# Performance work log

Measured on AMD Instinct MI355X. Metric: run time of the kernel, lower is better.

## Reference

```python
import jax, jax.numpy as jnp
import numpy as np

K = 500        # conv kernel == stride (non-overlapping windows)
C_IN = 8       # embedding dim
C_OUT = 128    # conv out channels
VOCAB = 257    # 256 byte values + padding idx 256


def setup_inputs() -> dict:
    key = jax.random.key(0)
    ks = jax.random.split(key, 10)
    B, L = 8, 1 << 20
    x = jax.random.randint(ks[0], (B, L), 0, VOCAB, dtype=jnp.int32)
    emb = 0.1 * jax.random.normal(ks[1], (VOCAB, C_IN), jnp.float32)
    emb = emb.at[VOCAB - 1].set(0.0)  # padding_idx=256 -> zero row
    lim_c = 1.0 / np.sqrt(C_IN * K)
    w1 = jax.random.uniform(ks[2], (C_OUT, C_IN, K), jnp.float32, -lim_c, lim_c)
    b1 = jax.random.uniform(ks[3], (C_OUT,), jnp.float32, -lim_c, lim_c)
    w2 = jax.random.uniform(ks[4], (C_OUT, C_IN, K), jnp.float32, -lim_c, lim_c)
    b2 = jax.random.uniform(ks[5], (C_OUT,), jnp.float32, -lim_c, lim_c)
    lim_d = 1.0 / np.sqrt(C_OUT)
    wd1 = jax.random.uniform(ks[6], (C_OUT, C_OUT), jnp.float32, -lim_d, lim_d)
    bd1 = jax.random.uniform(ks[7], (C_OUT,), jnp.float32, -lim_d, lim_d)
    wd2 = jax.random.uniform(ks[8], (1, C_OUT), jnp.float32, -lim_d, lim_d)
    bd2 = jax.random.uniform(ks[9], (1,), jnp.float32, -lim_d, lim_d)
    return {"x": x, "emb": emb, "w1": w1, "b1": b1, "w2": w2, "b2": b2,
            "wd1": wd1, "bd1": bd1, "wd2": wd2, "bd2": bd2}


def reference(x, emb, w1, b1, w2, b2, wd1, bd1, wd2, bd2):
    B, L = x.shape
    T = (L - K) // K + 1  # valid conv output length (== L // K here)
    xe = emb[x]                                  # [B, L, 8]  embedding lookup
    win = xe[:, : T * K].reshape(B, T, K, C_IN)  # [B, T, 500, 8] non-overlap windows
    c1 = jnp.einsum('btke,oek->bto', win, w1) + b1  # [B, T, 128]
    c2 = jnp.einsum('btke,oek->bto', win, w2) + b2
    gated = jax.nn.relu(c1) * jax.nn.sigmoid(c2)    # gated activation
    pooled = jnp.max(gated, axis=1)                 # global max pool over time -> [B, 128]
    h = jax.nn.relu(pooled @ wd1.T + bd1)           # [B, 128]
    out = jax.nn.sigmoid(h @ wd2.T + bd2)           # [B, 1]
    return out
```

## Files before the change

kernel.cpp:

```cpp
#include <hip/hip_runtime.h>

#define BATCH   8
#define LSEQ    1048576
#define KCONV   500
#define TWIN    2097
#define MROWS   16776
#define KDIM    4000
#define NDIM    256
#define COUT    128
#define VOCAB   257
#define VOCABP  256

#define BMR     80
#define NTILE   210
#define SLABP   20
#define NSLAB   25
#define NG      125
#define PLANE   (NDIM * 32)
#define AROWSH  168
#define STAGEN  (BMR * SLABP)

#define WTF_OFF   0ull
#define WTF_BYTES ((size_t)NG * PLANE * 2)
#define POOL_OFF  (WTF_OFF + WTF_BYTES)

typedef __attribute__((ext_vector_type(8))) __bf16 bf16x8;
typedef __attribute__((ext_vector_type(4))) float  floatx4;

__device__ inline unsigned short f2bf(float f) {
    union { float f; unsigned u; } c; c.f = f;
    return (unsigned short)((c.u + 0x7FFFu + ((c.u >> 16) & 1u)) >> 16);
}
__device__ inline unsigned pack2(float lo, float hi) {
    return (unsigned)f2bf(lo) | ((unsigned)f2bf(hi) << 16);
}

#define LDS_BARRIER() asm volatile("s_waitcnt lgkmcnt(0)\n\ts_barrier" ::: "memory")

__global__ __launch_bounds__(256) void wprep_kernel(const float* __restrict__ w1,
                                                    const float* __restrict__ w2,
                                                    unsigned short* __restrict__ Wtf,
                                                    float* __restrict__ pool) {
    const int n   = blockIdx.x;
    const int tid = threadIdx.x;
    __shared__ float tile[KDIM];
    const float* src = (n < COUT) ? (w1 + (size_t)n * KDIM)
                                  : (w2 + (size_t)(n - COUT) * KDIM);
    for (int i = tid; i < KDIM; i += 256) tile[i] = src[i];
    __syncthreads();
    for (int i = tid; i < KDIM; i += 256) {
        int g = i >> 5, kk = i & 31;
        Wtf[(size_t)g * PLANE + n * 32 + kk] = f2bf(tile[(i & 7) * KCONV + (i >> 3)]);
    }
    if (n == 0 && tid < BATCH * COUT / 2)
        ((float2*)pool)[tid] = float2{0.f, 0.f};
}

template<int ROWT, int RBASE>
__device__ __forceinline__ void gemm_path(
    const unsigned short* __restrict__ Wtf,
    const float* __restrict__ b1, const float* __restrict__ b2,
    float* __restrict__ pool,
    unsigned short* AsBase, const unsigned short* tableL,
    const int* const (&xptr)[4], const int (&loff)[4], const bool (&sval)[4],
    int tid, int m0)
{
    const int lane = tid & 63;
    const int r16  = lane & 15;
    const int q    = lane >> 4;
    const int cg   = (tid >> 6) & 3;

    const int o0 = cg * 32 + r16;
    const int o1 = o0 + 16;

    const size_t boff[4] = {
        (size_t)o0 * 32 + q * 8,
        (size_t)(o0 + 128) * 32 + q * 8,
        (size_t)o1 * 32 + q * 8,
        (size_t)(o1 + 128) * 32 + q * 8
    };

    floatx4 acc[ROWT][4];
#pragma unroll
    for (int i = 0; i < ROWT; ++i)
#pragma unroll
        for (int j = 0; j < 4; ++j) acc[i][j] = floatx4{0, 0, 0, 0};

    int xv[4], xn[4];
#pragma unroll
    for (int l = 0; l < 4; ++l) xv[l] = sval[l] ? xptr[l][0] : VOCABP;
    __syncthreads();

#pragma unroll
    for (int l = 0; l < 4; ++l) {
        if (l == 3 && tid >= STAGEN - 3 * 512) break;
        uint4 g = *(const uint4*)(tableL + xv[l] * 8);
        *(uint4*)(AsBase + loff[l]) = g;
    }
#pragma unroll
    for (int l = 0; l < 4; ++l) xv[l] = sval[l] ? xptr[l][SLABP] : VOCABP;
    LDS_BARRIER();

    bf16x8 bc0[4], bc1[4], bc2[4] = {};
#pragma unroll
    for (int j = 0; j < 4; ++j) {
        bc0[j] = *(const bf16x8*)(Wtf + boff[j]);
        bc1[j] = *(const bf16x8*)(Wtf + PLANE + boff[j]);
    }

    int buf = 0;
    for (int s = 0; s < NSLAB; ++s) {
        if (s + 2 < NSLAB) {
#pragma unroll
            for (int l = 0; l < 4; ++l)
                xn[l] = sval[l] ? xptr[l][(s + 2) * SLABP] : VOCABP;
        }

        const unsigned short* Asb = AsBase + buf * (BMR * AROWSH);
#pragma unroll
        for (int kt = 0; kt < 5; ++kt) {
            const int g = s * 5 + kt;
            if (g + 2 < NG) {
                const unsigned short* Wp = Wtf + (size_t)(g + 2) * PLANE;
#pragma unroll
                for (int j = 0; j < 4; ++j)
                    bc2[j] = *(const bf16x8*)(Wp + boff[j]);
            }
            bf16x8 af[ROWT];
#pragma unroll
            for (int i = 0; i < ROWT; ++i)
                af[i] = *(const bf16x8*)(Asb + ((RBASE + i) * 16 + r16) * AROWSH
                                         + (kt * 4 + q) * 8);
#pragma unroll
            for (int i = 0; i < ROWT; ++i) {
#pragma unroll
                for (int j = 0; j < 4; ++j)
                    acc[i][j] = __builtin_amdgcn_mfma_f32_16x16x32_bf16(
                        af[i], bc0[j], acc[i][j], 0, 0, 0);
            }
#pragma unroll
            for (int j = 0; j < 4; ++j) { bc0[j] = bc1[j]; bc1[j] = bc2[j]; }
        }

        if (s + 1 < NSLAB) {
            unsigned short* d = AsBase + (buf ^ 1) * (BMR * AROWSH);
#pragma unroll
            for (int l = 0; l < 4; ++l) {
                if (l == 3 && tid >= STAGEN - 3 * 512) break;
                uint4 g = *(const uint4*)(tableL + xv[l] * 8);
                *(uint4*)(d + loff[l]) = g;
            }
        }
#pragma unroll
        for (int l = 0; l < 4; ++l) xv[l] = xn[l];
        LDS_BARRIER();
        buf ^= 1;
    }

    const float b10 = b1[o0], b20 = b2[o0];
    const float b11 = b1[o1], b21 = b2[o1];
    float cur0 = 0.0f, cur1 = 0.0f;
    int curb = (m0 + RBASE * 16 + q * 4) / TWIN;
#pragma unroll
    for (int i = 0; i < ROWT; ++i) {
#pragma unroll
        for (int rg = 0; rg < 4; ++rg) {
            const int row = m0 + (RBASE + i) * 16 + q * 4 + rg;
            if (row < MROWS) {
                const int bb = row / TWIN;
                if (bb != curb) {
                    atomicMax((int*)&pool[curb * COUT + o0], __float_as_int(cur0));
                    atomicMax((int*)&pool[curb * COUT + o1], __float_as_int(cur1));
                    cur0 = 0.0f; cur1 = 0.0f; curb = bb;
                }
                {
                    const float c1 = acc[i][0][rg] + b10;
                    const float c2 = acc[i][1][rg] + b20;
                    cur0 = fmaxf(cur0, fmaxf(c1, 0.0f) / (1.0f + __expf(-c2)));
                }
                {
                    const float c1 = acc[i][2][rg] + b11;
                    const float c2 = acc[i][3][rg] + b21;
                    cur1 = fmaxf(cur1, fmaxf(c1, 0.0f) / (1.0f + __expf(-c2)));
                }
            }
        }
    }
    atomicMax((int*)&pool[curb * COUT + o0], __float_as_int(cur0));
    atomicMax((int*)&pool[curb * COUT + o1], __float_as_int(cur1));
}

__global__ __launch_bounds__(512) void gemm_kernel(const int* __restrict__ x,
                                                   const float* __restrict__ emb,
                                                   const unsigned short* __restrict__ Wtf,
                                                   const float* __restrict__ b1,
                                                   const float* __restrict__ b2,
                                                   float* __restrict__ pool) {
    __shared__ unsigned short tableL[VOCAB * 8];
    __shared__ unsigned short As[2][BMR * AROWSH];

    const int tid = threadIdx.x;
    const int m0  = blockIdx.x * BMR;

    if (tid < VOCAB) {
        const float4* er = (const float4*)(emb + tid * 8);
        float4 a = er[0], b = er[1];
        uint4 u;
        u.x = pack2(a.x, a.y); u.y = pack2(a.z, a.w);
        u.z = pack2(b.x, b.y); u.w = pack2(b.z, b.w);
        *(uint4*)(tableL + tid * 8) = u;
    }

    const int* xptr[4];
    int        loff[4];
    bool       sval[4];
#pragma unroll
    for (int l = 0; l < 4; ++l) {
        int idx = tid + 512 * l;
        sval[l] = (idx < STAGEN);
        int ic  = sval[l] ? idx : 0;
        int row = ic / SLABP;
        int pos = ic - row * SLABP;
        int am  = m0 + row;
        bool av = sval[l] && (am < MROWS);
        sval[l] = av;
        int amc = av ? am : 0;
        int b   = amc / TWIN;
        int t   = amc - b * TWIN;
        xptr[l] = x + ((size_t)b * LSEQ + (size_t)t * KCONV + pos);
        loff[l] = row * AROWSH + pos * 8;
    }

    if (tid < 256)
        gemm_path<3, 0>(Wtf, b1, b2, pool, (unsigned short*)As, tableL,
                        xptr, loff, sval, tid, m0);
    else
        gemm_path<2, 3>(Wtf, b1, b2, pool, (unsigned short*)As, tableL,
                        xptr, loff, sval, tid, m0);
}

__global__ __launch_bounds__(128) void head_kernel(const float* __restrict__ pool,
                                                   const float* __restrict__ wd1,
                                                   const float* __restrict__ bd1,
                                                   const float* __restrict__ wd2,
                                                   const float* __restrict__ bd2,
                                                   float* __restrict__ out) {
    __shared__ float red[BATCH][COUT];
    int j = threadIdx.x;
    float wj = wd2[j];
#pragma unroll
    for (int b = 0; b < BATCH; ++b) {
        float s = bd1[j];
        for (int i = 0; i < COUT; ++i) s += pool[b * COUT + i] * wd1[j * COUT + i];
        red[b][j] = fmaxf(s, 0.0f) * wj;
    }
    __syncthreads();
    if (j < BATCH) {
        float s = 0.0f;
        for (int i = 0; i < COUT; ++i) s += red[j][i];
        out[j] = 1.0f / (1.0f + expf(-(s + bd2[0])));
    }
}

extern "C" void kernel_launch(void* const* d_in, const int* in_sizes, int n_in,
                              void* d_out, int out_size, void* d_ws, size_t ws_size,
                              hipStream_t stream) {
    const int*   x   = (const int*)d_in[0];
    const float* emb = (const float*)d_in[1];
    const float* w1  = (const float*)d_in[2];
    const float* b1  = (const float*)d_in[3];
    const float* w2  = (const float*)d_in[4];
    const float* b2  = (const float*)d_in[5];
    const float* wd1 = (const float*)d_in[6];
    const float* bd1 = (const float*)d_in[7];
    const float* wd2 = (const float*)d_in[8];
    const float* bd2 = (const float*)d_in[9];
    float* out = (float*)d_out;

    unsigned short* Wtf  = (unsigned short*)((char*)d_ws + WTF_OFF);
    float*          pool = (float*)((char*)d_ws + POOL_OFF);

    wprep_kernel<<<dim3(NDIM), dim3(256), 0, stream>>>(w1, w2, Wtf, pool);
    gemm_kernel<<<dim3(NTILE), dim3(512), 0, stream>>>(x, emb, Wtf, b1, b2, pool);
    head_kernel<<<dim3(1), dim3(128), 0, stream>>>(pool, wd1, bd1, wd2, bd2, out);
}
```

Before: 190.8 us.

## Fuse head into GEMM via last-block counter and interleave LDS staging with MFMA

Removes the separate head kernel launch: each GEMM block atomically increments a counter, and the last block reads the pooled maxima and computes the dense head. The embedding-table staging of the next slab is spread across the MFMA k-steps instead of done as a block after them, so LDS traffic overlaps with matrix math. It also adds launch bounds with a minimum of 2 blocks per CU, which may constrain register allocation. The fused head relies on relaxed atomics and a vmcnt wait for ordering.

```diff
diff --git a/kernel.cpp b/kernel.cpp
--- a/kernel.cpp
+++ b/kernel.cpp
@@ -23,6 +23,7 @@
 #define WTF_OFF   0ull
 #define WTF_BYTES ((size_t)NG * PLANE * 2)
 #define POOL_OFF  (WTF_OFF + WTF_BYTES)
+#define CNT_OFF   (POOL_OFF + 4096)
 
 typedef __attribute__((ext_vector_type(8))) __bf16 bf16x8;
 typedef __attribute__((ext_vector_type(4))) float  floatx4;
@@ -40,7 +41,8 @@
 __global__ __launch_bounds__(256) void wprep_kernel(const float* __restrict__ w1,
                                                     const float* __restrict__ w2,
                                                     unsigned short* __restrict__ Wtf,
-                                                    float* __restrict__ pool) {
+                                                    float* __restrict__ pool,
+                                                    int* __restrict__ cnt) {
     const int n   = blockIdx.x;
     const int tid = threadIdx.x;
     __shared__ float tile[KDIM];
@@ -52,8 +54,10 @@
         int g = i >> 5, kk = i & 31;
         Wtf[(size_t)g * PLANE + n * 32 + kk] = f2bf(tile[(i & 7) * KCONV + (i >> 3)]);
     }
-    if (n == 0 && tid < BATCH * COUT / 2)
-        ((float2*)pool)[tid] = float2{0.f, 0.f};
+    if (n == 0) {
+        if (tid < 256) ((float4*)pool)[tid] = float4{0.f, 0.f, 0.f, 0.f};
+        if (tid == 0) *cnt = 0;
+    }
 }
 
 template<int ROWT, int RBASE>
@@ -63,7 +67,7 @@
     float* __restrict__ pool,
     unsigned short* AsBase, const unsigned short* tableL,
     const int* const (&xptr)[4], const int (&loff)[4], const bool (&sval)[4],
-    int tid, int m0)
+    const bool (&sact)[4], int tid, int m0)
 {
     const int lane = tid & 63;
     const int r16  = lane & 15;
@@ -93,9 +97,10 @@
 
 #pragma unroll
     for (int l = 0; l < 4; ++l) {
-        if (l == 3 && tid >= STAGEN - 3 * 512) break;
-        uint4 g = *(const uint4*)(tableL + xv[l] * 8);
-        *(uint4*)(AsBase + loff[l]) = g;
+        if (sact[l]) {
+            uint4 g = *(const uint4*)(tableL + xv[l] * 8);
+            *(uint4*)(AsBase + loff[l]) = g;
+        }
     }
 #pragma unroll
     for (int l = 0; l < 4; ++l) xv[l] = sval[l] ? xptr[l][SLABP] : VOCABP;
@@ -116,7 +121,11 @@
                 xn[l] = sval[l] ? xptr[l][(s + 2) * SLABP] : VOCABP;
         }
 
-        const unsigned short* Asb = AsBase + buf * (BMR * AROWSH);
+        const unsigned short* Asb  = AsBase + buf * (BMR * AROWSH);
+        unsigned short*       dstS = AsBase + (buf ^ 1) * (BMR * AROWSH);
+        const bool stg = (s + 1 < NSLAB);
+        uint4 gr[4];
+
 #pragma unroll
         for (int kt = 0; kt < 5; ++kt) {
             const int g = s * 5 + kt;
@@ -131,6 +140,10 @@
             for (int i = 0; i < ROWT; ++i)
                 af[i] = *(const bf16x8*)(Asb + ((RBASE + i) * 16 + r16) * AROWSH
                                          + (kt * 4 + q) * 8);
+
+            if (kt < 4 && stg && sact[kt])
+                gr[kt] = *(const uint4*)(tableL + xv[kt] * 8);
+
 #pragma unroll
             for (int i = 0; i < ROWT; ++i) {
 #pragma unroll
@@ -140,16 +153,9 @@
             }
 #pragma unroll
             for (int j = 0; j < 4; ++j) { bc0[j] = bc1[j]; bc1[j] = bc2[j]; }
-        }
-
-        if (s + 1 < NSLAB) {
-            unsigned short* d = AsBase + (buf ^ 1) * (BMR * AROWSH);
-#pragma unroll
-            for (int l = 0; l < 4; ++l) {
-                if (l == 3 && tid >= STAGEN - 3 * 512) break;
-                uint4 g = *(const uint4*)(tableL + xv[l] * 8);
-                *(uint4*)(d + loff[l]) = g;
-            }
+
+            if (kt >= 1 && stg && sact[kt - 1])
+                *(uint4*)(dstS + loff[kt - 1]) = gr[kt - 1];
         }
 #pragma unroll
         for (int l = 0; l < 4; ++l) xv[l] = xn[l];
@@ -190,14 +196,20 @@
     atomicMax((int*)&pool[curb * COUT + o1], __float_as_int(cur1));
 }
 
-__global__ __launch_bounds__(512) void gemm_kernel(const int* __restrict__ x,
-                                                   const float* __restrict__ emb,
-                                                   const unsigned short* __restrict__ Wtf,
-                                                   const float* __restrict__ b1,
-                                                   const float* __restrict__ b2,
-                                                   float* __restrict__ pool) {
-    __shared__ unsigned short tableL[VOCAB * 8];
-    __shared__ unsigned short As[2][BMR * AROWSH];
+__global__ __launch_bounds__(512, 2) void gemm_kernel(const int* __restrict__ x,
+                                                      const float* __restrict__ emb,
+                                                      const unsigned short* __restrict__ Wtf,
+                                                      const float* __restrict__ b1,
+                                                      const float* __restrict__ b2,
+                                                      float* __restrict__ pool,
+                                                      int* __restrict__ cnt,
+                                                      const float* __restrict__ wd1,
+                                                      const float* __restrict__ bd1,
+                                                      const float* __restrict__ wd2,
+                                                      const float* __restrict__ bd2,
+                                                      float* __restrict__ out) {
+    __shared__ __align__(16) unsigned short tableL[VOCAB * 8];
+    __shared__ __align__(16) unsigned short As[2][BMR * AROWSH];
 
     const int tid = threadIdx.x;
     const int m0  = blockIdx.x * BMR;
@@ -214,8 +226,10 @@
     const int* xptr[4];
     int        loff[4];
     bool       sval[4];
+    bool       sact[4];
 #pragma unroll
     for (int l = 0; l < 4; ++l) {
+        sact[l] = (l < 3) || (tid < STAGEN - 3 * 512);
         int idx = tid + 512 * l;
         sval[l] = (idx < STAGEN);
         int ic  = sval[l] ? idx : 0;
@@ -233,32 +247,44 @@
 
     if (tid < 256)
         gemm_path<3, 0>(Wtf, b1, b2, pool, (unsigned short*)As, tableL,
-                        xptr, loff, sval, tid, m0);
+                        xptr, loff, sval, sact, tid, m0);
     else
         gemm_path<2, 3>(Wtf, b1, b2, pool, (unsigned short*)As, tableL,
-                        xptr, loff, sval, tid, m0);
-}
-
-__global__ __launch_bounds__(128) void head_kernel(const float* __restrict__ pool,
-                                                   const float* __restrict__ wd1,
-                                                   const float* __restrict__ bd1,
-                                                   const float* __restrict__ wd2,
-                                                   const float* __restrict__ bd2,
-                                                   float* __restrict__ out) {
-    __shared__ float red[BATCH][COUT];
-    int j = threadIdx.x;
-    float wj = wd2[j];
-#pragma unroll
-    for (int b = 0; b < BATCH; ++b) {
-        float s = bd1[j];
-        for (int i = 0; i < COUT; ++i) s += pool[b * COUT + i] * wd1[j * COUT + i];
-        red[b][j] = fmaxf(s, 0.0f) * wj;
-    }
-    __syncthreads();
-    if (j < BATCH) {
+                        xptr, loff, sval, sact, tid, m0);
+
+    asm volatile("s_waitcnt vmcnt(0)" ::: "memory");
+    __syncthreads();
+    __shared__ int lastFlag;
+    if (tid == 0) {
+        int prev = __hip_atomic_fetch_add(cnt, 1, __ATOMIC_RELAXED, __HIP_MEMORY_SCOPE_AGENT);
+        lastFlag = (prev == NTILE - 1) ? 1 : 0;
+    }
+    __syncthreads();
+    if (!lastFlag) return;
+
+    float* poolL = (float*)As;
+    float* red   = poolL + BATCH * COUT;
+    poolL[tid] = __int_as_float(
+        __hip_atomic_load((int*)&pool[tid], __ATOMIC_RELAXED, __HIP_MEMORY_SCOPE_AGENT));
+    poolL[tid + 512] = __int_as_float(
+        __hip_atomic_load((int*)&pool[tid + 512], __ATOMIC_RELAXED, __HIP_MEMORY_SCOPE_AGENT));
+    __syncthreads();
+
+    if (tid < COUT) {
+        const int j = tid;
+        const float wj = wd2[j];
+#pragma unroll
+        for (int b = 0; b < BATCH; ++b) {
+            float s = bd1[j];
+            for (int i = 0; i < COUT; ++i) s += poolL[b * COUT + i] * wd1[j * COUT + i];
+            red[b * COUT + j] = fmaxf(s, 0.0f) * wj;
+        }
+    }
+    __syncthreads();
+    if (tid < BATCH) {
         float s = 0.0f;
-        for (int i = 0; i < COUT; ++i) s += red[j][i];
-        out[j] = 1.0f / (1.0f + expf(-(s + bd2[0])));
+        for (int i = 0; i < COUT; ++i) s += red[tid * COUT + i];
+        out[tid] = 1.0f / (1.0f + expf(-(s + bd2[0])));
     }
 }
 
@@ -279,8 +305,9 @@
 
     unsigned short* Wtf  = (unsigned short*)((char*)d_ws + WTF_OFF);
     float*          pool = (float*)((char*)d_ws + POOL_OFF);
-
-    wprep_kernel<<<dim3(NDIM), dim3(256), 0, stream>>>(w1, w2, Wtf, pool);
-    gemm_kernel<<<dim3(NTILE), dim3(512), 0, stream>>>(x, emb, Wtf, b1, b2, pool);
-    head_kernel<<<dim3(1), dim3(128), 0, stream>>>(pool, wd1, bd1, wd2, bd2, out);
-}
+    int*            cnt  = (int*)((char*)d_ws + CNT_OFF);
+
+    wprep_kernel<<<dim3(NDIM), dim3(256), 0, stream>>>(w1, w2, Wtf, pool, cnt);
+    gemm_kernel<<<dim3(NTILE), dim3(512), 0, stream>>>(x, emb, Wtf, b1, b2, pool, cnt,
+                                                       wd1, bd1, wd2, bd2, out);
+}
```

Measured after the change: 207.6 us. +8.8%, slower.
